# Kernel tuning notes

Hardware: AMD Instinct MI355X
Metric: run time of the kernel (lower is better)

The kernel has to match this reference:

```python
import jax, jax.numpy as jnp
import numpy as np

TAU = 1.0  # temperature of the NeuralSort relaxation


def _neural_sort(s, tau=TAU):
    """NeuralSort soft permutation matrix for scores s of shape (n,).
    Returns (n, n) row-stochastic matrix; row i ~ one-hot of i-th largest score."""
    n = s.shape[0]
    A_sum = jnp.abs(s[:, None] - s[None, :]).sum(-1)              # (n,)
    scaling = (n + 1 - 2 * jnp.arange(1, n + 1)).astype(s.dtype)  # (n,)
    scores = (scaling[:, None] * s[None, :] - A_sum[None, :]) / tau
    return jax.nn.softmax(scores, axis=-1)


def _soft_perm_gt(events, d):
    """Vectorized version of _get_soft_perm.
    events: (n,) int {0,1}; d: (n,) float durations. Returns (n, n) float32."""
    n = events.shape[0]
    idx = jnp.argsort(d)                 # ascending durations
    e_s = events[idx]                    # events in sorted order
    c = jnp.cumsum(e_s) - e_s            # exclusive event count before position i
    i = jnp.arange(n)
    lo = c                               # first allowed rank column
    hi = jnp.where(e_s == 1, i + 1, n)   # one past last allowed rank column
    j = jnp.arange(n)
    mask = (j[None, :] >= lo[:, None]) & (j[None, :] < hi[:, None])
    rows = mask.astype(jnp.float32) / (hi - lo)[:, None].astype(jnp.float32)
    inv = jnp.argsort(idx)               # perm_un_ascending @ M == rows re-indexed
    return rows[inv]


def _bce(p, y):
    # torch BCELoss: clamp log terms at -100, mean over all elements
    logp = jnp.maximum(jnp.log(p), -100.0)
    log1mp = jnp.maximum(jnp.log1p(-p), -100.0)
    return -(y * logp + (1.0 - y) * log1mp).mean()


def setup_inputs() -> dict:
    key = jax.random.key(0)
    k1, k2, k3 = jax.random.split(key, 3)
    n, C = 2048, 8
    logits = jax.random.normal(k1, (n, C), dtype=jnp.float32)
    durations = jax.random.uniform(k2, (n, C), dtype=jnp.float32)
    events = jax.random.randint(k3, (n, C), 0, 2).astype(jnp.int32)
    return {"logits": logits, "events": events, "durations": durations}


def reference(logits, events, durations):
    def col_loss(lh, e, d):
        p = _neural_sort(lh)        # (n, n) soft permutation prediction
        y = _soft_perm_gt(e, d)     # (n, n) soft permutation label
        return _bce(p, y)

    losses = jax.vmap(col_loss, in_axes=(1, 1, 1))(logits, events, durations)  # (C,)
    m = losses > 0
    denom = jnp.maximum(jnp.sum(m), 1).astype(losses.dtype)
    return jnp.sum(jnp.where(m, losses, 0.0)) / denom
```

## Files before the change

kernel.cpp:

```cpp
#include <hip/hip_runtime.h>
#include <hip/hip_bf16.h>
#include <math.h>

#define N 2048
#define NC 8


#if __has_builtin(__builtin_amdgcn_exp2f)
__device__ __forceinline__ float fexp2(float x) { return __builtin_amdgcn_exp2f(x); }
#else
__device__ __forceinline__ float fexp2(float x) { return exp2f(x); }
#endif
#if __has_builtin(__builtin_amdgcn_logf)
__device__ __forceinline__ float flog2(float x) { return __builtin_amdgcn_logf(x); }
#else
__device__ __forceinline__ float flog2(float x) { return log2f(x); }
#endif

#define INV_LN2 1.4426950408889634f
#define LN2_D   0.6931471805599453
#define CLAMP2  (-144.26950408889634f)

__global__ __launch_bounds__(256) void k_prep(const float* __restrict__ logits,
                                              const float* __restrict__ dur,
                                              const int* __restrict__ ev,
                                              float2* __restrict__ pack,
                                              int* __restrict__ lohi,
                                              double* __restrict__ acc,
                                              unsigned* __restrict__ counter) {
    __shared__ __align__(16) float s[N];
    __shared__ double part[256];
    __shared__ __align__(16) unsigned long long keys[N];
    __shared__ int pr[256], pv[256];

    int b = blockIdx.x;
    int tid = threadIdx.x;

    if (b == 0) {
        if (tid < 8) acc[tid] = 0.0;
        else if (tid == 8) counter[0] = 0u;
    }

    if (b < 512) {
        int col = b >> 6, chunk = b & 63;
        for (int k = 0; k < N / 256; ++k) {
            int i = tid + k * 256;
            s[i] = logits[i * NC + col];
        }
        __syncthreads();
        int jl = tid & 31, slice = tid >> 5;
        int j = chunk * 32 + jl;
        float sj = s[j];
        const float4* s4 = (const float4*)(s + slice * 256);
        double a0 = 0.0, a1 = 0.0, a2 = 0.0, a3 = 0.0;
        #pragma unroll 2
        for (int i = 0; i < 64; ++i) {
            float4 q = s4[i];
            a0 += (double)fabsf(sj - q.x);
            a1 += (double)fabsf(sj - q.y);
            a2 += (double)fabsf(sj - q.z);
            a3 += (double)fabsf(sj - q.w);
        }
        part[tid] = (a0 + a1) + (a2 + a3);
        __syncthreads();
        if (tid < 32) {
            double v = ((part[tid]       + part[tid + 32])  + (part[tid + 64]  + part[tid + 96])) +
                       ((part[tid + 128] + part[tid + 160]) + (part[tid + 192] + part[tid + 224]));
            pack[col * N + j] = make_float2(sj * INV_LN2, (float)v * INV_LN2);
        }
    } else {
        int b2 = b - 512;
        int col = b2 >> 6, chunk = b2 & 63;
        for (int k = 0; k < N / 256; ++k) {
            int i = tid + k * 256;
            unsigned int db = __float_as_uint(dur[i * NC + col]);
            int e = ev[i * NC + col];
            keys[i] = ((unsigned long long)db << 32) | (unsigned int)((i << 1) | e);
        }
        __syncthreads();
        int jl = tid & 31, slice = tid >> 5;
        int j = chunk * 32 + jl;
        unsigned long long kj = keys[j];
        const ulonglong2* k2 = (const ulonglong2*)(keys + slice * 256);
        int rank = 0, evlt = 0;
        #pragma unroll 2
        for (int i = 0; i < 128; ++i) {
            ulonglong2 kk = k2[i];
            int lt0 = (kk.x < kj) ? 1 : 0;
            rank += lt0;
            evlt += lt0 & (int)(kk.x & 1ull);
            int lt1 = (kk.y < kj) ? 1 : 0;
            rank += lt1;
            evlt += lt1 & (int)(kk.y & 1ull);
        }
        pr[tid] = rank;
        pv[tid] = evlt;
        __syncthreads();
        if (tid < 32) {
            int r = ((pr[tid]       + pr[tid + 32])  + (pr[tid + 64]  + pr[tid + 96])) +
                    ((pr[tid + 128] + pr[tid + 160]) + (pr[tid + 192] + pr[tid + 224]));
            int v = ((pv[tid]       + pv[tid + 32])  + (pv[tid + 64]  + pv[tid + 96])) +
                    ((pv[tid + 128] + pv[tid + 160]) + (pv[tid + 192] + pv[tid + 224]));
            int e = (int)(kj & 1ull);
            int hi = e ? (r + 1) : N;
            lohi[col * N + j] = v | (hi << 16);
        }
    }
}

__global__ __launch_bounds__(512) void k_bce(const float2* __restrict__ pack,
                                             const int* __restrict__ lohi,
                                             double* __restrict__ acc,
                                             unsigned* __restrict__ counter,
                                             float* __restrict__ out) {
    int col = blockIdx.x >> 6;
    int rg  = blockIdx.x & 63;
    __shared__ float4 sa4[N / 2];
    __shared__ double bsum[8];
    int tid = threadIdx.x;
    int wave = tid >> 6, lane = tid & 63;

    const float4* p4 = (const float4*)(pack + (size_t)col * N);
    #pragma unroll
    for (int k = 0; k < 2; ++k) {
        int i = tid + (k << 9);
        sa4[i] = p4[i];
    }
    __syncthreads();

    int row0 = (rg << 5) + (wave << 2);
    float sc0 = (float)(N - 1 - 2 * row0);

    int lh[4];
    #pragma unroll
    for (int c = 0; c < 4; ++c) lh[c] = lohi[col * N + row0 + c];

    float m = -INFINITY;
    #pragma unroll
    for (int k = 0; k < 16; ++k) {
        float4 q = sa4[lane + (k << 6)];
        float t0 = fmaf(sc0, q.x, -q.y);
        float t1 = fmaf(sc0, q.z, -q.w);
        m = fmaxf(m, fmaxf(t0, t1));
    }
    #pragma unroll
    for (int off = 32; off > 0; off >>= 1)
        m = fmaxf(m, __shfl_xor(m, off, 64));

    float se0 = 0.0f, se1 = 0.0f, se2 = 0.0f, se3 = 0.0f;
    #pragma unroll
    for (int k = 0; k < 16; ++k) {
        float4 q = sa4[lane + (k << 6)];
        {
            float g = fexp2(-(q.x + q.x));
            float E = fexp2(fmaf(sc0, q.x, -q.y) - m);
            se0 += E; E *= g;
            se1 += E; E *= g;
            se2 += E; E *= g;
            se3 += E;
        }
        {
            float g = fexp2(-(q.z + q.z));
            float E = fexp2(fmaf(sc0, q.z, -q.w) - m);
            se0 += E; E *= g;
            se1 += E; E *= g;
            se2 += E; E *= g;
            se3 += E;
        }
    }
    #pragma unroll
    for (int off = 32; off > 0; off >>= 1) {
        se0 += __shfl_xor(se0, off, 64);
        se1 += __shfl_xor(se1, off, 64);
        se2 += __shfl_xor(se2, off, 64);
        se3 += __shfl_xor(se3, off, 64);
    }
    float se[4] = {se0, se1, se2, se3};

    float C2v[4], yv[4];
    unsigned lo[4], wl[4];
    double rbase = 0.0;
    #pragma unroll
    for (int c = 0; c < 4; ++c) {
        float L2 = flog2(se[c]);
        rbase -= 2048.0 * (double)L2;
        C2v[c] = CLAMP2 + L2;
        lo[c] = (unsigned)(lh[c] & 0xffff);
        wl[c] = (unsigned)((lh[c] >> 16) & 0xffff) - lo[c];
        yv[c] = 1.0f / (float)wl[c];
    }

    float a1[4] = {0.0f, 0.0f, 0.0f, 0.0f};
    float a2[4] = {0.0f, 0.0f, 0.0f, 0.0f};
    #pragma unroll
    for (int k = 0; k < 16; ++k) {
        float4 q = sa4[lane + (k << 6)];
        int j0 = (lane + (k << 6)) << 1;
        {
            float tsv = q.x + q.x;
            float g = fexp2(-tsv);
            float x = fmaf(sc0, q.x, -q.y) - m;
            float E = fexp2(x);
            #pragma unroll
            for (int c = 0; c < 4; ++c) {
                float mx2 = fmaxf(flog2(se[c] - E), C2v[c]);
                a1[c] += mx2;
                float mx1 = fmaxf(x, C2v[c]);
                float w = ((unsigned)(j0 - lo[c]) < wl[c]) ? (mx1 - mx2) : 0.0f;
                a2[c] += w;
                E *= g;
                x -= tsv;
            }
        }
        {
            float tsv = q.z + q.z;
            float g = fexp2(-tsv);
            float x = fmaf(sc0, q.z, -q.w) - m;
            float E = fexp2(x);
            #pragma unroll
            for (int c = 0; c < 4; ++c) {
                float mx2 = fmaxf(flog2(se[c] - E), C2v[c]);
                a1[c] += mx2;
                float mx1 = fmaxf(x, C2v[c]);
                float w = ((unsigned)(j0 + 1 - lo[c]) < wl[c]) ? (mx1 - mx2) : 0.0f;
                a2[c] += w;
                E *= g;
                x -= tsv;
            }
        }
    }
    float r = 0.0f;
    #pragma unroll
    for (int c = 0; c < 4; ++c) r += fmaf(yv[c], a2[c], a1[c]);
    #pragma unroll
    for (int off = 32; off > 0; off >>= 1)
        r += __shfl_xor(r, off, 64);

    if (lane == 0) bsum[wave] = rbase + (double)r;
    __syncthreads();
    if (tid == 0) {
        double tot = ((bsum[0] + bsum[1]) + (bsum[2] + bsum[3])) +
                     ((bsum[4] + bsum[5]) + (bsum[6] + bsum[7]));
        atomicAdd(&acc[col], LN2_D * tot);
        __threadfence();
        unsigned old = atomicAdd(counter, 1u);
        if (old == (unsigned)(NC * 64 - 1)) {
            __threadfence();
            float ssum = 0.0f;
            int cnt = 0;
            for (int c = 0; c < NC; ++c) {
                double av2 = atomicAdd(&acc[c], 0.0);
                float lc = (float)(-av2 / ((double)N * (double)N));
                if (lc > 0.0f) { ssum += lc; cnt++; }
            }
            out[0] = ssum / (float)(cnt > 0 ? cnt : 1);
        }
    }
}

extern "C" void kernel_launch(void* const* d_in, const int* in_sizes, int n_in,
                              void* d_out, int out_size, void* d_ws, size_t ws_size,
                              hipStream_t stream) {
    const float* logits    = (const float*)d_in[0];
    const int*   events    = (const int*)d_in[1];
    const float* durations = (const float*)d_in[2];
    float* out = (float*)d_out;

    char* ws = (char*)d_ws;
    double*   acc     = (double*)ws;
    float2*   pack    = (float2*)(ws + 64);
    int*      lohi    = (int*)(ws + 64 + (size_t)NC * N * sizeof(float2));
    unsigned* counter = (unsigned*)(ws + 64 + (size_t)NC * N * (sizeof(float2) + sizeof(int)));

    k_prep<<<dim3(1024), 256, 0, stream>>>(logits, durations, events, pack, lohi, acc, counter);
    k_bce<<<dim3(NC * 64), 512, 0, stream>>>(pack, lohi, acc, counter, out);
}
```

Before: 96.75 us.

## Sort scores per column and skip underflowing softmax chunks per wavefront

The prep kernel now computes each score's rank within its column and scatters the packed (s, A_sum) pairs into sorted order, keeping the original column index alongside. In the BCE kernel, chunks where every lane's exponent underflows to zero are detected with a wave-wide vote. For those chunks the exp2/log2 work is skipped and log(se - E) is replaced by log(se). Sorting clusters the negligible terms so that whole wavefronts can take the cheap path. The cost is extra comparisons in prep, an extra index array in LDS, and added branching.

```diff
diff --git a/kernel.cpp b/kernel.cpp
--- a/kernel.cpp
+++ b/kernel.cpp
@@ -24,12 +24,14 @@
 __global__ __launch_bounds__(256) void k_prep(const float* __restrict__ logits,
                                               const float* __restrict__ dur,
                                               const int* __restrict__ ev,
-                                              float2* __restrict__ pack,
+                                              float2* __restrict__ psort,
+                                              unsigned short* __restrict__ origj,
                                               int* __restrict__ lohi,
                                               double* __restrict__ acc,
                                               unsigned* __restrict__ counter) {
     __shared__ __align__(16) float s[N];
     __shared__ double part[256];
+    __shared__ int pri[256];
     __shared__ __align__(16) unsigned long long keys[N];
     __shared__ int pr[256], pv[256];
 
@@ -52,21 +54,32 @@
         int j = chunk * 32 + jl;
         float sj = s[j];
         const float4* s4 = (const float4*)(s + slice * 256);
+        int ib = slice * 256;
         double a0 = 0.0, a1 = 0.0, a2 = 0.0, a3 = 0.0;
+        int rk = 0;
         #pragma unroll 2
         for (int i = 0; i < 64; ++i) {
             float4 q = s4[i];
+            int i0 = ib + 4 * i;
             a0 += (double)fabsf(sj - q.x);
             a1 += (double)fabsf(sj - q.y);
             a2 += (double)fabsf(sj - q.z);
             a3 += (double)fabsf(sj - q.w);
+            rk += ((int)(q.x < sj)) | (((int)(q.x == sj)) & (int)(i0 + 0 < j));
+            rk += ((int)(q.y < sj)) | (((int)(q.y == sj)) & (int)(i0 + 1 < j));
+            rk += ((int)(q.z < sj)) | (((int)(q.z == sj)) & (int)(i0 + 2 < j));
+            rk += ((int)(q.w < sj)) | (((int)(q.w == sj)) & (int)(i0 + 3 < j));
         }
         part[tid] = (a0 + a1) + (a2 + a3);
+        pri[tid] = rk;
         __syncthreads();
         if (tid < 32) {
             double v = ((part[tid]       + part[tid + 32])  + (part[tid + 64]  + part[tid + 96])) +
                        ((part[tid + 128] + part[tid + 160]) + (part[tid + 192] + part[tid + 224]));
-            pack[col * N + j] = make_float2(sj * INV_LN2, (float)v * INV_LN2);
+            int r = ((pri[tid]       + pri[tid + 32])  + (pri[tid + 64]  + pri[tid + 96])) +
+                    ((pri[tid + 128] + pri[tid + 160]) + (pri[tid + 192] + pri[tid + 224]));
+            psort[col * N + r] = make_float2(sj * INV_LN2, (float)v * INV_LN2);
+            origj[col * N + r] = (unsigned short)j;
         }
     } else {
         int b2 = b - 512;
@@ -108,7 +121,8 @@
     }
 }
 
-__global__ __launch_bounds__(512) void k_bce(const float2* __restrict__ pack,
+__global__ __launch_bounds__(512) void k_bce(const float2* __restrict__ psort,
+                                             const unsigned short* __restrict__ origj,
                                              const int* __restrict__ lohi,
                                              double* __restrict__ acc,
                                              unsigned* __restrict__ counter,
@@ -116,15 +130,18 @@
     int col = blockIdx.x >> 6;
     int rg  = blockIdx.x & 63;
     __shared__ float4 sa4[N / 2];
+    __shared__ unsigned sow[N / 2];
     __shared__ double bsum[8];
     int tid = threadIdx.x;
     int wave = tid >> 6, lane = tid & 63;
 
-    const float4* p4 = (const float4*)(pack + (size_t)col * N);
+    const float4* p4 = (const float4*)(psort + (size_t)col * N);
+    const unsigned* g4 = (const unsigned*)(origj + (size_t)col * N);
     #pragma unroll
     for (int k = 0; k < 2; ++k) {
         int i = tid + (k << 9);
         sa4[i] = p4[i];
+        sow[i] = g4[i];
     }
     __syncthreads();
 
@@ -147,13 +164,20 @@
     for (int off = 32; off > 0; off >>= 1)
         m = fmaxf(m, __shfl_xor(m, off, 64));
 
+    unsigned skipmask = 0u;
     float se0 = 0.0f, se1 = 0.0f, se2 = 0.0f, se3 = 0.0f;
     #pragma unroll
     for (int k = 0; k < 16; ++k) {
         float4 q = sa4[lane + (k << 6)];
+        float Ea = fexp2(fmaf(sc0, q.x, -q.y) - m);
+        float Eb = fexp2(fmaf(sc0, q.z, -q.w) - m);
+        if (__all((Ea == 0.0f) & (Eb == 0.0f))) {
+            skipmask |= (1u << k);
+            continue;
+        }
         {
             float g = fexp2(-(q.x + q.x));
-            float E = fexp2(fmaf(sc0, q.x, -q.y) - m);
+            float E = Ea;
             se0 += E; E *= g;
             se1 += E; E *= g;
             se2 += E; E *= g;
@@ -161,7 +185,7 @@
         }
         {
             float g = fexp2(-(q.z + q.z));
-            float E = fexp2(fmaf(sc0, q.z, -q.w) - m);
+            float E = Eb;
             se0 += E; E *= g;
             se1 += E; E *= g;
             se2 += E; E *= g;
@@ -177,12 +201,13 @@
     }
     float se[4] = {se0, se1, se2, se3};
 
-    float C2v[4], yv[4];
+    float L2v[4], C2v[4], yv[4];
     unsigned lo[4], wl[4];
     double rbase = 0.0;
     #pragma unroll
     for (int c = 0; c < 4; ++c) {
         float L2 = flog2(se[c]);
+        L2v[c] = L2;
         rbase -= 2048.0 * (double)L2;
         C2v[c] = CLAMP2 + L2;
         lo[c] = (unsigned)(lh[c] & 0xffff);
@@ -195,37 +220,65 @@
     #pragma unroll
     for (int k = 0; k < 16; ++k) {
         float4 q = sa4[lane + (k << 6)];
-        int j0 = (lane + (k << 6)) << 1;
-        {
-            float tsv = q.x + q.x;
-            float g = fexp2(-tsv);
-            float x = fmaf(sc0, q.x, -q.y) - m;
-            float E = fexp2(x);
-            #pragma unroll
-            for (int c = 0; c < 4; ++c) {
-                float mx2 = fmaxf(flog2(se[c] - E), C2v[c]);
-                a1[c] += mx2;
-                float mx1 = fmaxf(x, C2v[c]);
-                float w = ((unsigned)(j0 - lo[c]) < wl[c]) ? (mx1 - mx2) : 0.0f;
-                a2[c] += w;
-                E *= g;
-                x -= tsv;
-            }
-        }
-        {
-            float tsv = q.z + q.z;
-            float g = fexp2(-tsv);
-            float x = fmaf(sc0, q.z, -q.w) - m;
-            float E = fexp2(x);
-            #pragma unroll
-            for (int c = 0; c < 4; ++c) {
-                float mx2 = fmaxf(flog2(se[c] - E), C2v[c]);
-                a1[c] += mx2;
-                float mx1 = fmaxf(x, C2v[c]);
-                float w = ((unsigned)(j0 + 1 - lo[c]) < wl[c]) ? (mx1 - mx2) : 0.0f;
-                a2[c] += w;
-                E *= g;
-                x -= tsv;
+        unsigned ow = sow[lane + (k << 6)];
+        int ja = (int)(ow & 0xffffu), jb = (int)(ow >> 16);
+        if ((skipmask >> k) & 1u) {
+            {
+                float tsv = q.x + q.x;
+                float x = fmaf(sc0, q.x, -q.y) - m;
+                #pragma unroll
+                for (int c = 0; c < 4; ++c) {
+                    a1[c] += L2v[c];
+                    float mx1 = fmaxf(x, C2v[c]);
+                    float w = ((unsigned)(ja - lo[c]) < wl[c]) ? (mx1 - L2v[c]) : 0.0f;
+                    a2[c] += w;
+                    x -= tsv;
+                }
+            }
+            {
+                float tsv = q.z + q.z;
+                float x = fmaf(sc0, q.z, -q.w) - m;
+                #pragma unroll
+                for (int c = 0; c < 4; ++c) {
+                    a1[c] += L2v[c];
+                    float mx1 = fmaxf(x, C2v[c]);
+                    float w = ((unsigned)(jb - lo[c]) < wl[c]) ? (mx1 - L2v[c]) : 0.0f;
+                    a2[c] += w;
+                    x -= tsv;
+                }
+            }
+        } else {
+            {
+                float tsv = q.x + q.x;
+                float g = fexp2(-tsv);
+                float x = fmaf(sc0, q.x, -q.y) - m;
+                float E = fexp2(x);
+                #pragma unroll
+                for (int c = 0; c < 4; ++c) {
+                    float mx2 = fmaxf(flog2(se[c] - E), C2v[c]);
+                    a1[c] += mx2;
+                    float mx1 = fmaxf(x, C2v[c]);
+                    float w = ((unsigned)(ja - lo[c]) < wl[c]) ? (mx1 - mx2) : 0.0f;
+                    a2[c] += w;
+                    E *= g;
+                    x -= tsv;
+                }
+            }
+            {
+                float tsv = q.z + q.z;
+                float g = fexp2(-tsv);
+                float x = fmaf(sc0, q.z, -q.w) - m;
+                float E = fexp2(x);
+                #pragma unroll
+                for (int c = 0; c < 4; ++c) {
+                    float mx2 = fmaxf(flog2(se[c] - E), C2v[c]);
+                    a1[c] += mx2;
+                    float mx1 = fmaxf(x, C2v[c]);
+                    float w = ((unsigned)(jb - lo[c]) < wl[c]) ? (mx1 - mx2) : 0.0f;
+                    a2[c] += w;
+                    E *= g;
+                    x -= tsv;
+                }
             }
         }
     }
@@ -267,11 +320,12 @@
     float* out = (float*)d_out;
 
     char* ws = (char*)d_ws;
-    double*   acc     = (double*)ws;
-    float2*   pack    = (float2*)(ws + 64);
-    int*      lohi    = (int*)(ws + 64 + (size_t)NC * N * sizeof(float2));
-    unsigned* counter = (unsigned*)(ws + 64 + (size_t)NC * N * (sizeof(float2) + sizeof(int)));
-
-    k_prep<<<dim3(1024), 256, 0, stream>>>(logits, durations, events, pack, lohi, acc, counter);
-    k_bce<<<dim3(NC * 64), 512, 0, stream>>>(pack, lohi, acc, counter, out);
+    double*         acc     = (double*)ws;
+    float2*         psort   = (float2*)(ws + 64);
+    int*            lohi    = (int*)(ws + 64 + (size_t)NC * N * sizeof(float2));
+    unsigned*       counter = (unsigned*)(ws + 64 + (size_t)NC * N * (sizeof(float2) + sizeof(int)));
+    unsigned short* origj   = (unsigned short*)(ws + 64 + (size_t)NC * N * (sizeof(float2) + sizeof(int)) + 64);
+
+    k_prep<<<dim3(1024), 256, 0, stream>>>(logits, durations, events, psort, origj, lohi, acc, counter);
+    k_bce<<<dim3(NC * 64), 512, 0, stream>>>(psort, origj, lohi, acc, counter, out);
 }
```

Result: faster. 91.65 us (-5.3%).
